# Kernel tuning notes

Hardware: AMD Instinct MI355X
Metric: run time of the kernel (lower is better)

## Reference

```python
import jax, jax.numpy as jnp
import numpy as np

B, N = 16, 500                 # N == max_objs, so object k -> anno row k
NUM_CLASSES = 10
GRID = 1440
OSF = 4                        # out_size_factor
FM = GRID // OSF               # 360x360 feature map
VOX = 0.075
PCR0 = -54.0                   # point_cloud_range x/y min
MIN_OVERLAP = 0.1
MIN_RADIUS = 2
R_MAX = 12                     # static cap on gaussian radius (dims<=5m -> r<=~7)


def setup_inputs():
    key = jax.random.key(0)
    k1, k2, k3, k4, k5, k6 = jax.random.split(key, 6)
    xy = jax.random.uniform(k1, (B, N, 2), minval=-50.0, maxval=50.0)
    z = jax.random.uniform(k2, (B, N, 1), minval=-3.0, maxval=1.0)
    dims = jax.random.uniform(k3, (B, N, 3), minval=1.0, maxval=5.0)  # w, l, h > 0
    vel = jax.random.normal(k4, (B, N, 2))
    rot = jax.random.uniform(k5, (B, N, 1), minval=-np.pi, maxval=np.pi)
    gt_bboxes_3d = jnp.concatenate([xy, z, dims, vel, rot], axis=-1)  # [B,N,9]
    gt_labels_3d = jax.random.randint(k6, (B, N), 1, NUM_CLASSES + 1)  # 1-based
    return {"gt_bboxes_3d": gt_bboxes_3d, "gt_labels_3d": gt_labels_3d}


def gaussian_radius(height, width, min_overlap):
    # CenterNet/mmdet3d gaussian_radius, vectorized
    b1 = height + width
    c1 = width * height * (1 - min_overlap) / (1 + min_overlap)
    r1 = (b1 + jnp.sqrt(b1 ** 2 - 4 * c1)) / 2
    b2 = 2 * (height + width)
    c2 = (1 - min_overlap) * width * height
    r2 = (b2 + jnp.sqrt(b2 ** 2 - 16 * c2)) / 2
    a3 = 4 * min_overlap
    b3 = -2 * min_overlap * (height + width)
    c3 = (min_overlap - 1) * width * height
    r3 = (b3 + jnp.sqrt(b3 ** 2 - 4 * a3 * c3)) / 2
    return jnp.minimum(jnp.minimum(r1, r2), r3)


def _targets(boxes, labels):
    # Per-class torch.where + concat within the single task == stable sort by label
    order = jnp.argsort(labels, axis=1, stable=True)
    boxes = jnp.take_along_axis(boxes, order[..., None], axis=1)
    labels = jnp.take_along_axis(labels, order, axis=1)
    cls_id = labels - 1                                    # [B,N]

    x, y, z = boxes[..., 0], boxes[..., 1], boxes[..., 2]
    w, l, h = boxes[..., 3], boxes[..., 4], boxes[..., 5]
    rot = boxes[..., 8]

    wp = w / VOX / OSF   # width in feature-map pixels
    lp = l / VOX / OSF   # length in feature-map pixels
    cx_f = (x - PCR0) / VOX / OSF
    cy_f = (y - PCR0) / VOX / OSF
    cx = cx_f.astype(jnp.int32)   # trunc, matches .to(torch.int32)
    cy = cy_f.astype(jnp.int32)

    valid = (wp > 0) & (lp > 0) & (cx >= 0) & (cx < FM) & (cy >= 0) & (cy < FM)

    r = gaussian_radius(lp, wp, MIN_OVERLAP)               # note (length, width)
    radius = jnp.maximum(MIN_RADIUS, jnp.floor(r).astype(jnp.int32))  # [B,N]
    sigma = (2 * radius.astype(boxes.dtype) + 1) / 6.0

    # Gaussian window scatter-max (draw_umich_gaussian)
    off = jnp.arange(-R_MAX, R_MAX + 1)
    dyg, dxg = jnp.meshgrid(off, off, indexing="ij")       # [Wn,Wn]
    d2 = (dxg ** 2 + dyg ** 2).astype(boxes.dtype)
    g = jnp.exp(-d2[None, None] / (2 * sigma[..., None, None] ** 2))  # [B,N,Wn,Wn]
    rb = radius[..., None, None]
    wmask = (jnp.abs(dxg) <= rb) & (jnp.abs(dyg) <= rb)    # 2r+1 window
    yy = cy[..., None, None] + dyg
    xx = cx[..., None, None] + dxg
    ok = valid[..., None, None] & wmask & (yy >= 0) & (yy < FM) & (xx >= 0) & (xx < FM)
    flat_idx = jnp.where(ok, cls_id[..., None, None] * FM * FM + yy * FM + xx, -1)
    vals = jnp.where(ok, g, 0.0)

    def scat(idx, v):
        return jnp.zeros(NUM_CLASSES * FM * FM, boxes.dtype).at[idx.ravel()].max(
            v.ravel(), mode="drop")

    heatmap = jax.vmap(scat)(flat_idx, vals).reshape(B, NUM_CLASSES, FM, FM)

    # anno_box: [dx, dy, z, log(w), log(l), log(h), sin(rot), cos(rot)]
    anno = jnp.concatenate([
        jnp.stack([cx_f - cx, cy_f - cy, z], axis=-1),
        jnp.log(jnp.stack([w, l, h], axis=-1)),
        jnp.sin(rot)[..., None],
        jnp.cos(rot)[..., None],
    ], axis=-1)                                            # [B,N,8]
    anno = jnp.where(valid[..., None], anno, 0.0)
    ind = jnp.where(valid, cy * FM + cx, 0).astype(jnp.int32)
    mask = valid.astype(jnp.uint8)
    return heatmap, anno, ind, mask


def reference(gt_bboxes_3d, gt_labels_3d):
    return _targets(gt_bboxes_3d, gt_labels_3d)
```

## Files before the change

### kernel.cpp

```cpp
#include <hip/hip_runtime.h>

constexpr int B_ = 16;
constexpr int N_ = 500;
constexpr int NC = 10;
constexpr int FM_ = 360;
constexpr int RMAXC = 12;
constexpr long HM_ELEMS = (long)B_ * NC * FM_ * FM_;
constexpr long ANNO_OFF = HM_ELEMS;
constexpr long IND_OFF  = ANNO_OFF + (long)B_ * N_ * 8;
constexpr long MASK_OFF = IND_OFF + (long)B_ * N_;

constexpr int PREP_BLKS = 32;
constexpr int ZERO_BLKS = 2048;

struct ObjParams {
    float cx_f, cy_f, sigma;
    int cx, cy, radius;
    bool valid;
};

__device__ inline ObjParams compute_params(const float* bx) {
    float x = bx[0], y = bx[1];
    float w = bx[3], l = bx[4];
    ObjParams o;
    float wp = w / 0.075f / 4.0f;
    float lp = l / 0.075f / 4.0f;
    o.cx_f = (x + 54.0f) / 0.075f / 4.0f;
    o.cy_f = (y + 54.0f) / 0.075f / 4.0f;
    o.cx = (int)o.cx_f;
    o.cy = (int)o.cy_f;
    o.valid = (wp > 0.0f) && (lp > 0.0f) &&
              (o.cx >= 0) && (o.cx < FM_) && (o.cy >= 0) && (o.cy < FM_);
    float height = lp, width = wp;
    float b1 = height + width;
    float c1 = width * height * 0.9f / 1.1f;
    float r1 = (b1 + sqrtf(b1 * b1 - 4.0f * c1)) / 2.0f;
    float b2 = 2.0f * (height + width);
    float c2 = 0.9f * width * height;
    float r2 = (b2 + sqrtf(b2 * b2 - 16.0f * c2)) / 2.0f;
    float b3 = -0.2f * (height + width);
    float c3 = -0.9f * width * height;
    float r3 = (b3 + sqrtf(b3 * b3 - 1.6f * c3)) / 2.0f;
    float r = fminf(fminf(r1, r2), r3);
    o.radius = max(2, (int)floorf(r));
    o.sigma = (2.0f * (float)o.radius + 1.0f) / 6.0f;
    return o;
}

__global__ __launch_bounds__(256) void prep_zero_kernel(
        const float* __restrict__ boxes, const int* __restrict__ labels,
        float* __restrict__ out) {
    int blk = blockIdx.x;
    int tid = threadIdx.x;

    if (blk < PREP_BLKS) {
        int b = blk >> 1;
        int half = blk & 1;
        __shared__ int lab[N_];
        for (int k = tid; k < N_; k += 256) lab[k] = labels[b * N_ + k];
        __syncthreads();
        int i = half * 250 + tid;
        if (tid < 250) {
            int c = lab[i];
            int rank = 0;
            #pragma unroll 8
            for (int j = 0; j < N_; ++j) {
                int lj = lab[j];
                rank += (lj < c) | ((lj == c) & (j < i));
            }
            const float* bx = boxes + (long)(b * N_ + i) * 9;
            ObjParams o = compute_params(bx);
            float* anno = out + ANNO_OFF + (long)(b * N_ + rank) * 8;
            if (o.valid) {
                float zz = bx[2], w = bx[3], l = bx[4], h = bx[5], rot = bx[8];
                float4 a0 = {o.cx_f - (float)o.cx, o.cy_f - (float)o.cy, zz, logf(w)};
                float4 a1 = {logf(l), logf(h), sinf(rot), cosf(rot)};
                *(float4*)anno = a0;
                *(float4*)(anno + 4) = a1;
                out[IND_OFF + b * N_ + rank]  = (float)(o.cy * FM_ + o.cx);
                out[MASK_OFF + b * N_ + rank] = 1.0f;
            } else {
                float4 z = {0.f, 0.f, 0.f, 0.f};
                *(float4*)anno = z;
                *(float4*)(anno + 4) = z;
                out[IND_OFF + b * N_ + rank]  = 0.0f;
                out[MASK_OFF + b * N_ + rank] = 0.0f;
            }
        }
    } else {
        int zblk = blk - PREP_BLKS;
        float4* hm4 = (float4*)out;
        constexpr int n4 = (int)(HM_ELEMS / 4);
        float4 z = {0.f, 0.f, 0.f, 0.f};
        for (int k = zblk * 256 + tid; k < n4; k += ZERO_BLKS * 256) hm4[k] = z;
    }
}

__global__ __launch_bounds__(256) void scatter_kernel(
        const float* __restrict__ boxes, const int* __restrict__ labels,
        float* __restrict__ out) {
    int obj = blockIdx.x * 4 + (threadIdx.x >> 6);
    int lane = threadIdx.x & 63;
    const float* bx = boxes + (long)obj * 9;
    ObjParams o = compute_params(bx);
    if (!o.valid) return;
    int b = obj / N_;
    int cls = labels[obj] - 1;
    int reff = min(o.radius, RMAXC);
    int wsz = 2 * reff + 1;
    int total = wsz * wsz;
    float denom = 2.0f * (o.sigma * o.sigma);
    float* hm = out + ((long)b * NC + cls) * FM_ * FM_;
    for (int c = lane; c < total; c += 64) {
        int q = c / wsz;
        int dy = q - reff;
        int dx = c - q * wsz - reff;
        int yy = o.cy + dy, xx = o.cx + dx;
        if (yy < 0 || yy >= FM_ || xx < 0 || xx >= FM_) continue;
        float d2 = (float)(dx * dx + dy * dy);
        float g = expf(-d2 / denom);
        atomicMax((int*)&hm[yy * FM_ + xx], __float_as_int(g));
    }
}

extern "C" void kernel_launch(void* const* d_in, const int* in_sizes, int n_in,
                              void* d_out, int out_size, void* d_ws, size_t ws_size,
                              hipStream_t stream) {
    const float* boxes = (const float*)d_in[0];
    const int* labels  = (const int*)d_in[1];
    float* out = (float*)d_out;

    prep_zero_kernel<<<PREP_BLKS + ZERO_BLKS, 256, 0, stream>>>(boxes, labels, out);
    scatter_kernel<<<(B_ * N_) / 4, 256, 0, stream>>>(boxes, labels, out);
}
```

Before: 30.85 us.

## Replace zero-fill plus atomic scatter with single-pass per-stripe gather heatmap

Replaces the heatmap zero-fill and atomicMax scatter kernels with one gather kernel. Each block owns an 8-row stripe of one batch/class plane, collects the overlapping objects into shared memory, and writes every heatmap element exactly once with float4 stores. This removes a kernel launch, the separate zero pass and the global atomics. In exchange, each block recomputes object parameters for all 500 boxes, and every pixel loops over the stripe's object list.

```diff
diff --git a/kernel.cpp b/kernel.cpp
--- a/kernel.cpp
+++ b/kernel.cpp
@@ -10,8 +10,10 @@
 constexpr long IND_OFF  = ANNO_OFF + (long)B_ * N_ * 8;
 constexpr long MASK_OFF = IND_OFF + (long)B_ * N_;
 
+constexpr int ROWS = 8;
+constexpr int STRIPES = FM_ / ROWS;
+constexpr int GATHER_BLKS = B_ * NC * STRIPES;
 constexpr int PREP_BLKS = 32;
-constexpr int ZERO_BLKS = 2048;
 
 struct ObjParams {
     float cx_f, cy_f, sigma;
@@ -47,15 +49,71 @@
     return o;
 }
 
-__global__ __launch_bounds__(256) void prep_zero_kernel(
+__global__ __launch_bounds__(256) void fused_gather_kernel(
         const float* __restrict__ boxes, const int* __restrict__ labels,
         float* __restrict__ out) {
     int blk = blockIdx.x;
     int tid = threadIdx.x;
 
-    if (blk < PREP_BLKS) {
-        int b = blk >> 1;
-        int half = blk & 1;
+    if (blk < GATHER_BLKS) {
+        int b = blk / (NC * STRIPES);
+        int rem = blk - b * (NC * STRIPES);
+        int c = rem / STRIPES;
+        int stripe = rem - c * STRIPES;
+        int y0 = stripe * ROWS;
+
+        __shared__ int s_cnt;
+        __shared__ int s_cx[N_], s_cy[N_], s_re[N_];
+        __shared__ float s_den[N_];
+        if (tid == 0) s_cnt = 0;
+        __syncthreads();
+
+        for (int k = tid; k < N_; k += 256) {
+            if (labels[b * N_ + k] - 1 != c) continue;
+            const float* bx = boxes + (long)(b * N_ + k) * 9;
+            ObjParams o = compute_params(bx);
+            if (!o.valid) continue;
+            int reff = min(o.radius, RMAXC);
+            if (o.cy + reff < y0 || o.cy - reff > y0 + ROWS - 1) continue;
+            int p = atomicAdd(&s_cnt, 1);
+            s_cx[p] = o.cx;
+            s_cy[p] = o.cy;
+            s_re[p] = reff;
+            s_den[p] = 2.0f * (o.sigma * o.sigma);
+        }
+        __syncthreads();
+        int n = s_cnt;
+
+        float4* base4 = (float4*)(out + (((long)(b * NC + c)) * FM_ + y0) * FM_);
+        constexpr int NF4 = ROWS * FM_ / 4;
+        for (int k = tid; k < NF4; k += 256) {
+            int row = k / 90;
+            int y = y0 + row;
+            int x0 = (k - row * 90) * 4;
+            float4 acc = {0.f, 0.f, 0.f, 0.f};
+            for (int j = 0; j < n; ++j) {
+                int dy = y - s_cy[j];
+                int re = s_re[j];
+                if (dy > re || dy < -re) continue;
+                int cxj = s_cx[j];
+                float den = s_den[j];
+                float fdy2 = (float)(dy * dy);
+                #pragma unroll
+                for (int i = 0; i < 4; ++i) {
+                    int dx = x0 + i - cxj;
+                    if (dx > re || dx < -re) continue;
+                    float d2 = (float)(dx * dx) + fdy2;
+                    float g = expf(-d2 / den);
+                    float* a = (float*)&acc + i;
+                    *a = fmaxf(*a, g);
+                }
+            }
+            base4[k] = acc;
+        }
+    } else {
+        int blk2 = blk - GATHER_BLKS;
+        int b = blk2 >> 1;
+        int half = blk2 & 1;
         __shared__ int lab[N_];
         for (int k = tid; k < N_; k += 256) lab[k] = labels[b * N_ + k];
         __syncthreads();
@@ -87,39 +145,6 @@
                 out[MASK_OFF + b * N_ + rank] = 0.0f;
             }
         }
-    } else {
-        int zblk = blk - PREP_BLKS;
-        float4* hm4 = (float4*)out;
-        constexpr int n4 = (int)(HM_ELEMS / 4);
-        float4 z = {0.f, 0.f, 0.f, 0.f};
-        for (int k = zblk * 256 + tid; k < n4; k += ZERO_BLKS * 256) hm4[k] = z;
-    }
-}
-
-__global__ __launch_bounds__(256) void scatter_kernel(
-        const float* __restrict__ boxes, const int* __restrict__ labels,
-        float* __restrict__ out) {
-    int obj = blockIdx.x * 4 + (threadIdx.x >> 6);
-    int lane = threadIdx.x & 63;
-    const float* bx = boxes + (long)obj * 9;
-    ObjParams o = compute_params(bx);
-    if (!o.valid) return;
-    int b = obj / N_;
-    int cls = labels[obj] - 1;
-    int reff = min(o.radius, RMAXC);
-    int wsz = 2 * reff + 1;
-    int total = wsz * wsz;
-    float denom = 2.0f * (o.sigma * o.sigma);
-    float* hm = out + ((long)b * NC + cls) * FM_ * FM_;
-    for (int c = lane; c < total; c += 64) {
-        int q = c / wsz;
-        int dy = q - reff;
-        int dx = c - q * wsz - reff;
-        int yy = o.cy + dy, xx = o.cx + dx;
-        if (yy < 0 || yy >= FM_ || xx < 0 || xx >= FM_) continue;
-        float d2 = (float)(dx * dx + dy * dy);
-        float g = expf(-d2 / denom);
-        atomicMax((int*)&hm[yy * FM_ + xx], __float_as_int(g));
     }
 }
 
@@ -130,6 +155,6 @@
     const int* labels  = (const int*)d_in[1];
     float* out = (float*)d_out;
 
-    prep_zero_kernel<<<PREP_BLKS + ZERO_BLKS, 256, 0, stream>>>(boxes, labels, out);
-    scatter_kernel<<<(B_ * N_) / 4, 256, 0, stream>>>(boxes, labels, out);
+    fused_gather_kernel<<<GATHER_BLKS + PREP_BLKS, 256, 0, stream>>>(
+        boxes, labels, out);
 }
```

Measured after the change: 51.73 us. 1.68x slower.

## Replace global atomic scatter with per-band shared-memory heatmap tiles

Applied to the files above, without the earlier changes.

The prep kernel now sorts objects by class, records per-class start offsets and packs per-object splat parameters into workspace. A new gather kernel assigns each block one 15-row band of one class plane, zeroes a shared-memory tile, splats every overlapping object with shared atomics, and writes the band out once. This removes the separate global zero pass and the global atomicMax traffic. In exchange each block loops over all objects of its class, and 54KB of shared memory per block limits occupancy.

```diff
diff --git a/kernel.cpp b/kernel.cpp
--- a/kernel.cpp
+++ b/kernel.cpp
@@ -10,8 +10,11 @@
 constexpr long IND_OFF  = ANNO_OFF + (long)B_ * N_ * 8;
 constexpr long MASK_OFF = IND_OFF + (long)B_ * N_;
 
-constexpr int PREP_BLKS = 32;
-constexpr int ZERO_BLKS = 2048;
+constexpr int BAND = 15;
+constexpr int NBANDS = FM_ / BAND;
+constexpr int GB_BLKS = B_ * NC * NBANDS;
+
+constexpr size_t WSPAR_OFF = 1024;
 
 struct ObjParams {
     float cx_f, cy_f, sigma;
@@ -47,80 +50,111 @@
     return o;
 }
 
-__global__ __launch_bounds__(256) void prep_zero_kernel(
+__global__ __launch_bounds__(256) void prep_kernel(
         const float* __restrict__ boxes, const int* __restrict__ labels,
+        float* __restrict__ out, int* __restrict__ wsStart,
+        int4* __restrict__ wsPar) {
+    int blk = blockIdx.x;
+    int tid = threadIdx.x;
+    int b = blk >> 1;
+    int half = blk & 1;
+    __shared__ int lab[N_];
+    for (int k = tid; k < N_; k += 256) lab[k] = labels[b * N_ + k];
+    __syncthreads();
+
+    if (half == 0 && tid <= NC) {
+        int t = tid, cnt = 0;
+        for (int j = 0; j < N_; ++j) cnt += ((lab[j] - 1) < t);
+        wsStart[b * (NC + 1) + t] = cnt;
+    }
+
+    int i = half * 250 + tid;
+    if (tid < 250) {
+        int c = lab[i];
+        int rank = 0;
+        #pragma unroll 8
+        for (int j = 0; j < N_; ++j) {
+            int lj = lab[j];
+            rank += (lj < c) | ((lj == c) & (j < i));
+        }
+        const float* bx = boxes + (long)(b * N_ + i) * 9;
+        ObjParams o = compute_params(bx);
+
+        int4 rec;
+        rec.x = o.cx;
+        rec.y = o.cy;
+        rec.z = o.valid ? min(o.radius, RMAXC) : -1;
+        rec.w = __float_as_int(1.0f / (2.0f * (o.sigma * o.sigma)));
+        wsPar[b * N_ + rank] = rec;
+
+        float* anno = out + ANNO_OFF + (long)(b * N_ + rank) * 8;
+        if (o.valid) {
+            float zz = bx[2], w = bx[3], l = bx[4], h = bx[5], rot = bx[8];
+            float4 a0 = {o.cx_f - (float)o.cx, o.cy_f - (float)o.cy, zz, logf(w)};
+            float4 a1 = {logf(l), logf(h), sinf(rot), cosf(rot)};
+            *(float4*)anno = a0;
+            *(float4*)(anno + 4) = a1;
+            out[IND_OFF + b * N_ + rank]  = (float)(o.cy * FM_ + o.cx);
+            out[MASK_OFF + b * N_ + rank] = 1.0f;
+        } else {
+            float4 z = {0.f, 0.f, 0.f, 0.f};
+            *(float4*)anno = z;
+            *(float4*)(anno + 4) = z;
+            out[IND_OFF + b * N_ + rank]  = 0.0f;
+            out[MASK_OFF + b * N_ + rank] = 0.0f;
+        }
+    }
+}
+
+__global__ __launch_bounds__(256) void gather_kernel(
+        const int* __restrict__ wsStart, const int4* __restrict__ wsPar,
         float* __restrict__ out) {
     int blk = blockIdx.x;
     int tid = threadIdx.x;
+    int b = blk / (NC * NBANDS);
+    int rem = blk - b * (NC * NBANDS);
+    int c = rem / NBANDS;
+    int y0 = (rem - c * NBANDS) * BAND;
 
-    if (blk < PREP_BLKS) {
-        int b = blk >> 1;
-        int half = blk & 1;
-        __shared__ int lab[N_];
-        for (int k = tid; k < N_; k += 256) lab[k] = labels[b * N_ + k];
-        __syncthreads();
-        int i = half * 250 + tid;
-        if (tid < 250) {
-            int c = lab[i];
-            int rank = 0;
-            #pragma unroll 8
-            for (int j = 0; j < N_; ++j) {
-                int lj = lab[j];
-                rank += (lj < c) | ((lj == c) & (j < i));
-            }
-            const float* bx = boxes + (long)(b * N_ + i) * 9;
-            ObjParams o = compute_params(bx);
-            float* anno = out + ANNO_OFF + (long)(b * N_ + rank) * 8;
-            if (o.valid) {
-                float zz = bx[2], w = bx[3], l = bx[4], h = bx[5], rot = bx[8];
-                float4 a0 = {o.cx_f - (float)o.cx, o.cy_f - (float)o.cy, zz, logf(w)};
-                float4 a1 = {logf(l), logf(h), sinf(rot), cosf(rot)};
-                *(float4*)anno = a0;
-                *(float4*)(anno + 4) = a1;
-                out[IND_OFF + b * N_ + rank]  = (float)(o.cy * FM_ + o.cx);
-                out[MASK_OFF + b * N_ + rank] = 1.0f;
-            } else {
-                float4 z = {0.f, 0.f, 0.f, 0.f};
-                *(float4*)anno = z;
-                *(float4*)(anno + 4) = z;
-                out[IND_OFF + b * N_ + rank]  = 0.0f;
-                out[MASK_OFF + b * N_ + rank] = 0.0f;
-            }
+    __shared__ int tile[BAND * FM_];
+    __shared__ int4 s_rec[N_];
+
+    int start = wsStart[b * (NC + 1) + c];
+    int end   = wsStart[b * (NC + 1) + c + 1];
+    int cnt = end - start;
+    for (int k = tid; k < cnt; k += 256) s_rec[k] = wsPar[b * N_ + start + k];
+    constexpr int NT4 = BAND * FM_ / 4;
+    int4 z4 = {0, 0, 0, 0};
+    for (int k = tid; k < NT4; k += 256) ((int4*)tile)[k] = z4;
+    __syncthreads();
+
+    for (int j = 0; j < cnt; ++j) {
+        int4 r = s_rec[j];
+        int re = r.z;
+        if (re < 0) continue;
+        int cy = r.y;
+        int rlo = max(y0, cy - re), rhi = min(y0 + BAND - 1, cy + re);
+        if (rlo > rhi) continue;
+        int cx = r.x;
+        float inv = __int_as_float(r.w);
+        int wsz = 2 * re + 1;
+        int cellsP = (rhi - rlo + 1) << 5;
+        for (int cell = tid; cell < cellsP; cell += 256) {
+            int row = cell >> 5;
+            int dxi = cell & 31;
+            if (dxi >= wsz) continue;
+            int dx = dxi - re;
+            int x = cx + dx;
+            if (x < 0 || x >= FM_) continue;
+            int dy = rlo + row - cy;
+            float g = expf(-(float)(dx * dx + dy * dy) * inv);
+            atomicMax(&tile[(rlo - y0 + row) * FM_ + x], __float_as_int(g));
         }
-    } else {
-        int zblk = blk - PREP_BLKS;
-        float4* hm4 = (float4*)out;
-        constexpr int n4 = (int)(HM_ELEMS / 4);
-        float4 z = {0.f, 0.f, 0.f, 0.f};
-        for (int k = zblk * 256 + tid; k < n4; k += ZERO_BLKS * 256) hm4[k] = z;
     }
-}
+    __syncthreads();
 
-__global__ __launch_bounds__(256) void scatter_kernel(
-        const float* __restrict__ boxes, const int* __restrict__ labels,
-        float* __restrict__ out) {
-    int obj = blockIdx.x * 4 + (threadIdx.x >> 6);
-    int lane = threadIdx.x & 63;
-    const float* bx = boxes + (long)obj * 9;
-    ObjParams o = compute_params(bx);
-    if (!o.valid) return;
-    int b = obj / N_;
-    int cls = labels[obj] - 1;
-    int reff = min(o.radius, RMAXC);
-    int wsz = 2 * reff + 1;
-    int total = wsz * wsz;
-    float denom = 2.0f * (o.sigma * o.sigma);
-    float* hm = out + ((long)b * NC + cls) * FM_ * FM_;
-    for (int c = lane; c < total; c += 64) {
-        int q = c / wsz;
-        int dy = q - reff;
-        int dx = c - q * wsz - reff;
-        int yy = o.cy + dy, xx = o.cx + dx;
-        if (yy < 0 || yy >= FM_ || xx < 0 || xx >= FM_) continue;
-        float d2 = (float)(dx * dx + dy * dy);
-        float g = expf(-d2 / denom);
-        atomicMax((int*)&hm[yy * FM_ + xx], __float_as_int(g));
-    }
+    float4* base4 = (float4*)(out + (((long)(b * NC + c)) * FM_ + y0) * FM_);
+    for (int k = tid; k < NT4; k += 256) base4[k] = ((float4*)tile)[k];
 }
 
 extern "C" void kernel_launch(void* const* d_in, const int* in_sizes, int n_in,
@@ -129,7 +163,9 @@
     const float* boxes = (const float*)d_in[0];
     const int* labels  = (const int*)d_in[1];
     float* out = (float*)d_out;
+    int* wsStart = (int*)d_ws;
+    int4* wsPar = (int4*)((char*)d_ws + WSPAR_OFF);
 
-    prep_zero_kernel<<<PREP_BLKS + ZERO_BLKS, 256, 0, stream>>>(boxes, labels, out);
-    scatter_kernel<<<(B_ * N_) / 4, 256, 0, stream>>>(boxes, labels, out);
+    prep_kernel<<<2 * B_, 256, 0, stream>>>(boxes, labels, out, wsStart, wsPar);
+    gather_kernel<<<GB_BLKS, 256, 0, stream>>>(wsStart, wsPar, out);
 }
```

Result: slower. 54.60 us (+77.0%).
